# Kernel optimization log

Measured on AMD Instinct MI355X. Metric: run time of the kernel, lower is better.

## Reference

```python
import jax, jax.numpy as jnp
import numpy as np

IN_CH, IN_U, OUT_CH, OUT_U = 1152, 8, 10, 16
BATCH = 256
ROUTING_EPOCH = 3


def squash(s, axis=-1):
    # v = (||s||^2 / (1 + ||s||^2)) * s / ||s||
    sqn = jnp.sum(s * s, axis=axis, keepdims=True)
    return s * (sqn / ((1.0 + sqn) * jnp.sqrt(sqn + 1e-9)))


def setup_inputs() -> dict:
    key = jax.random.key(0)
    k1, k2 = jax.random.split(key)
    inp = jax.random.normal(k1, (BATCH, IN_CH, IN_U), dtype=jnp.float32)
    W = jax.random.normal(k2, (IN_CH, OUT_CH, OUT_U, IN_U), dtype=jnp.float32)
    return {"inp": inp, "W": W}


def reference(inp, W):
    # u_hat[b,i,o,u] = sum_k W[i,o,u,k] * inp[b,i,k]   -> [B, 1152, 10, 16]
    u_hat = jnp.einsum('iouk,bik->biou', W, inp)
    B = inp.shape[0]
    b = jnp.zeros((IN_CH, OUT_CH), dtype=inp.dtype)  # routing logits [1152, 10]
    v = None
    for _ in range(ROUTING_EPOCH):
        c = jax.nn.softmax(b, axis=1)                 # [1152, 10]
        s = jnp.einsum('biou,io->bou', u_hat, c)      # sum over input capsules -> [B, 10, 16]
        v = squash(s, axis=-1)                        # [B, 10, 16]
        # delta_b[i,o] = mean_b sum_u u_hat[b,i,o,u] * v[b,o,u]
        b = b + jnp.einsum('biou,bou->io', u_hat, v) / B
    return v  # == original v.squeeze(): [B, 10, 16]
```

## Files before the change

### kernel.cpp

```cpp
#include <hip/hip_runtime.h>
#include <math.h>

#define NB 256
#define IC 1152
#define OC 10
#define OU 16
#define IK 8
#define KTOT (IC * IK)
#define NTOT (OC * OU)
#define S_KS 16

typedef __attribute__((ext_vector_type(8))) short short8;
typedef __attribute__((ext_vector_type(4))) float f32x4;

static __device__ __forceinline__ unsigned short f2bf(float f) {
    unsigned u = __float_as_uint(f);
    unsigned r = (u + 0x7FFF + ((u >> 16) & 1)) >> 16;
    return (unsigned short)r;
}

__global__ __launch_bounds__(256) void prep_kernel(
    const float* __restrict__ inp,
    float* __restrict__ blog,
    unsigned short* __restrict__ inpb,
    unsigned short* __restrict__ inpT)
{
    const int kt  = blockIdx.x;
    const int bt  = blockIdx.y;
    const int tid = threadIdx.x;

    {
        int bid = blockIdx.y * 144 + blockIdx.x;
        if (bid < 45) blog[bid * 256 + tid] = 0.f;
    }

    __shared__ unsigned short sh[64][65];

#pragma unroll
    for (int j = 0; j < 4; ++j) {
        int q     = j * 256 + tid;
        int b_loc = q >> 4;
        int kq    = (q & 15) * 4;
        float4 g = *(const float4*)&inp[(size_t)(bt * 64 + b_loc) * KTOT + kt * 64 + kq];
        unsigned short h0 = f2bf(g.x), h1 = f2bf(g.y), h2 = f2bf(g.z), h3 = f2bf(g.w);
        sh[kq][b_loc] = h0; sh[kq + 1][b_loc] = h1;
        sh[kq + 2][b_loc] = h2; sh[kq + 3][b_loc] = h3;
        short4 pk = { (short)h0, (short)h1, (short)h2, (short)h3 };
        *(short4*)&inpb[(size_t)(bt * 64 + b_loc) * KTOT + kt * 64 + kq] = pk;
    }
    __syncthreads();

#pragma unroll
    for (int j = 0; j < 4; ++j) {
        int q     = j * 256 + tid;
        int k_loc = q >> 4;
        int b4    = (q & 15) * 4;
        short4 pk = { (short)sh[k_loc][b4],     (short)sh[k_loc][b4 + 1],
                      (short)sh[k_loc][b4 + 2], (short)sh[k_loc][b4 + 3] };
        *(short4*)&inpT[(size_t)(kt * 64 + k_loc) * 256 + bt * 64 + b4] = pk;
    }
}

#define BLP 584
__global__ __launch_bounds__(256) void spass_kernel(
    const unsigned short* __restrict__ inpb,
    const float* __restrict__ W,
    const float* __restrict__ blog,
    float* __restrict__ part)
{
    const int bid  = blockIdx.x;
    const int nt   = bid % 10;
    const int ks   = (bid / 10) % 16;
    const int mtg  = bid / 160;
    const int tid  = threadIdx.x;
    const int w    = tid >> 6;
    const int lane = tid & 63;
    const int l15  = lane & 15;
    const int koff = (lane >> 4) * 8;
    const int k0   = ks * 576;
    const int i0   = ks * 72;
    const int mt   = mtg * 4 + w;

    __shared__ unsigned short Bl[16 * BLP];
    __shared__ float c_loc[72];

    if (tid < 72) {
        const float* br = &blog[(size_t)(i0 + tid) * OC];
        float x[OC], m = -1e30f;
#pragma unroll
        for (int o = 0; o < OC; ++o) { x[o] = br[o]; m = fmaxf(m, x[o]); }
        float ssum = 0.f;
#pragma unroll
        for (int o = 0; o < OC; ++o) ssum += expf(x[o] - m);
        c_loc[tid] = expf(x[nt] - m) / ssum;
    }
    __syncthreads();

#pragma unroll
    for (int jj = 0; jj < 5; ++jj) {
        int q = jj * 256 + tid;
        if (q < 1152) {
            int i_loc = q >> 4, u = q & 15;
            const float* wr = W + (((size_t)(i0 + i_loc) * OC + nt) * OU + u) * IK;
            float4 a = *(const float4*)wr;
            float4 b = *(const float4*)(wr + 4);
            float cc = c_loc[i_loc];
            union { short8 v; unsigned short us[8]; } pk;
            pk.us[0] = f2bf(cc * a.x); pk.us[1] = f2bf(cc * a.y);
            pk.us[2] = f2bf(cc * a.z); pk.us[3] = f2bf(cc * a.w);
            pk.us[4] = f2bf(cc * b.x); pk.us[5] = f2bf(cc * b.y);
            pk.us[6] = f2bf(cc * b.z); pk.us[7] = f2bf(cc * b.w);
            *(short8*)&Bl[u * BLP + i_loc * 8] = pk.v;
        }
    }
    __syncthreads();

    const unsigned short* ap  = inpb + (size_t)(mt * 16 + l15) * KTOT + k0 + koff;
    const unsigned short* bls = &Bl[l15 * BLP + koff];

    f32x4 acc = {0.f, 0.f, 0.f, 0.f};
#pragma unroll
    for (int kk = 0; kk < 18; ++kk) {
        short8 av = *(const short8*)(ap + kk * 32);
        short8 bv = *(const short8*)(bls + kk * 32);
        acc = __builtin_amdgcn_mfma_f32_16x16x32_bf16(av, bv, acc, 0, 0, 0);
    }

    float* pp = part + ((size_t)ks * NB + mt * 16 + (lane >> 4) * 4) * NTOT + nt * 16 + l15;
#pragma unroll
    for (int r = 0; r < 4; ++r)
        pp[(size_t)r * NTOT] = acc[r];
}

__global__ __launch_bounds__(256) void reduce_squash_kernel(
    const float* __restrict__ part, float* __restrict__ vout,
    unsigned short* __restrict__ vT)
{
    const int tid = threadIdx.x;
    const int el  = tid & 31;
    const int kl  = tid >> 5;
    const int e   = blockIdx.x * 32 + el;

    float a = part[(size_t)(kl * 2) * (NB * NTOT) + e]
            + part[(size_t)(kl * 2 + 1) * (NB * NTOT) + e];

    __shared__ float red[8][36];
    red[kl][el] = a;
    __syncthreads();

    if (tid < 32) {
        float s = ((red[0][el] + red[1][el]) + (red[2][el] + red[3][el]))
                + ((red[4][el] + red[5][el]) + (red[6][el] + red[7][el]));
        float sq = s * s;
        sq += __shfl_xor(sq, 1);
        sq += __shfl_xor(sq, 2);
        sq += __shfl_xor(sq, 4);
        sq += __shfl_xor(sq, 8);
        float vv = s * (sq / ((1.f + sq) * sqrtf(sq + 1e-9f)));
        vout[e] = vv;
        int n = e % NTOT, b = e / NTOT;
        vT[(size_t)n * 256 + b] = f2bf(vv);
    }
}

__global__ __launch_bounds__(256) void delta_kernel(
    const unsigned short* __restrict__ inpT,
    const unsigned short* __restrict__ vT,
    const float* __restrict__ W,
    float* __restrict__ blog)
{
    const int g    = blockIdx.x * 4 + (threadIdx.x >> 6);
    const int lane = threadIdx.x & 63;
    const int mt   = g % 576;
    const int nt   = g / 576;
    const int l15  = lane & 15;
    const int quad = lane >> 4;
    const int koff = quad * 8;

    const unsigned short* ap = inpT + (size_t)(mt * 16 + l15) * 256 + koff;
    const unsigned short* bp = vT   + (size_t)(nt * 16 + l15) * 256 + koff;

    f32x4 acc = {0.f, 0.f, 0.f, 0.f};
#pragma unroll
    for (int kk = 0; kk < 8; ++kk) {
        short8 av = *(const short8*)(ap + kk * 32);
        short8 bv = *(const short8*)(bp + kk * 32);
        acc = __builtin_amdgcn_mfma_f32_16x16x32_bf16(av, bv, acc, 0, 0, 0);
    }

    const int i = mt * 2 + (quad >> 1);
    const float* wr = W + (((size_t)i * OC + nt) * OU + l15) * IK + (quad & 1) * 4;
    float4 wf = *(const float4*)wr;
    float wsum = wf.x * acc[0] + wf.y * acc[1] + wf.z * acc[2] + wf.w * acc[3];

    wsum += __shfl_xor(wsum, 16);
    wsum += __shfl_xor(wsum, 1);
    wsum += __shfl_xor(wsum, 2);
    wsum += __shfl_xor(wsum, 4);
    wsum += __shfl_xor(wsum, 8);

    if ((lane & 31) == 0)
        blog[(size_t)i * OC + nt] += wsum * (1.0f / NB);
}

extern "C" void kernel_launch(void* const* d_in, const int* in_sizes, int n_in,
                              void* d_out, int out_size, void* d_ws, size_t ws_size,
                              hipStream_t stream) {
    const float* inp = (const float*)d_in[0];
    const float* W   = (const float*)d_in[1];
    float* vout = (float*)d_out;

    float* blog = (float*)d_ws;
    float* part = blog + IC * OC;
    unsigned short* inpb = (unsigned short*)(part + (size_t)S_KS * NB * NTOT);
    unsigned short* inpT = inpb + (size_t)NB * KTOT;
    unsigned short* vT   = inpT + (size_t)KTOT * 256;

    prep_kernel<<<dim3(144, 4), dim3(256), 0, stream>>>(inp, blog, inpb, inpT);

    for (int t = 0; t < 3; ++t) {
        spass_kernel<<<dim3(640), dim3(256), 0, stream>>>(inpb, W, blog, part);
        reduce_squash_kernel<<<dim3(NB * NTOT / 32), dim3(256), 0, stream>>>(part, vout, vT);
        if (t < 2)
            delta_kernel<<<dim3(1440), dim3(256), 0, stream>>>(inpT, vT, W, blog);
    }
}
```

Baseline: 132.8 us.

## Fuse partial-sum reduction and squash into delta kernel for first two iterations

The delta kernel now reduces the split-K partial sums, applies squash, and builds the bf16 transposed v tile in shared memory itself, for its own output-capsule slice. This removes two reduce/squash launches and the global vT round trip. In exchange, each of the 36 blocks per output capsule recomputes the same reduction and squash, so part is read redundantly. Blocks grow to 1024 threads with extra shared memory.

```diff
diff --git a/kernel.cpp b/kernel.cpp
--- a/kernel.cpp
+++ b/kernel.cpp
@@ -133,8 +133,7 @@
 }
 
 __global__ __launch_bounds__(256) void reduce_squash_kernel(
-    const float* __restrict__ part, float* __restrict__ vout,
-    unsigned short* __restrict__ vT)
+    const float* __restrict__ part, float* __restrict__ vout)
 {
     const int tid = threadIdx.x;
     const int el  = tid & 31;
@@ -156,29 +155,69 @@
         sq += __shfl_xor(sq, 2);
         sq += __shfl_xor(sq, 4);
         sq += __shfl_xor(sq, 8);
-        float vv = s * (sq / ((1.f + sq) * sqrtf(sq + 1e-9f)));
-        vout[e] = vv;
-        int n = e % NTOT, b = e / NTOT;
-        vT[(size_t)n * 256 + b] = f2bf(vv);
-    }
-}
-
-__global__ __launch_bounds__(256) void delta_kernel(
+        vout[e] = s * (sq / ((1.f + sq) * sqrtf(sq + 1e-9f)));
+    }
+}
+
+__global__ __launch_bounds__(1024) void delta_fused_kernel(
+    const float* __restrict__ part,
     const unsigned short* __restrict__ inpT,
-    const unsigned short* __restrict__ vT,
     const float* __restrict__ W,
     float* __restrict__ blog)
 {
-    const int g    = blockIdx.x * 4 + (threadIdx.x >> 6);
-    const int lane = threadIdx.x & 63;
-    const int mt   = g % 576;
-    const int nt   = g / 576;
+    const int mtg = blockIdx.x;
+    const int nt  = blockIdx.y;
+    const int tid = threadIdx.x;
+
+    __shared__ float sred[256][17];
+    __shared__ float alpha[256];
+    __shared__ unsigned short vT_loc[16][264];
+
+    {
+        const int nl = tid & 15;
+        const int bq = tid >> 4;
+#pragma unroll
+        for (int rep = 0; rep < 4; ++rep) {
+            int b = bq + rep * 64;
+            const float* pp = part + (size_t)b * NTOT + nt * 16 + nl;
+            float s = 0.f;
+#pragma unroll
+            for (int ks = 0; ks < S_KS; ++ks)
+                s += pp[(size_t)ks * (NB * NTOT)];
+            sred[b][nl] = s;
+        }
+    }
+    __syncthreads();
+
+    if (tid < 256) {
+        const int b = tid;
+        float sq = 0.f;
+#pragma unroll
+        for (int u = 0; u < 16; ++u) { float x = sred[b][u]; sq += x * x; }
+        alpha[b] = sq / ((1.f + sq) * sqrtf(sq + 1e-9f));
+    }
+    __syncthreads();
+
+    {
+        const int nl = tid & 15;
+        const int bq = tid >> 4;
+#pragma unroll
+        for (int rep = 0; rep < 4; ++rep) {
+            int b = bq + rep * 64;
+            vT_loc[nl][b] = f2bf(sred[b][nl] * alpha[b]);
+        }
+    }
+    __syncthreads();
+
+    const int w    = tid >> 6;
+    const int lane = tid & 63;
+    const int mt   = mtg * 16 + w;
     const int l15  = lane & 15;
     const int quad = lane >> 4;
     const int koff = quad * 8;
 
     const unsigned short* ap = inpT + (size_t)(mt * 16 + l15) * 256 + koff;
-    const unsigned short* bp = vT   + (size_t)(nt * 16 + l15) * 256 + koff;
+    const unsigned short* bp = &vT_loc[l15][koff];
 
     f32x4 acc = {0.f, 0.f, 0.f, 0.f};
 #pragma unroll
@@ -214,14 +253,13 @@
     float* part = blog + IC * OC;
     unsigned short* inpb = (unsigned short*)(part + (size_t)S_KS * NB * NTOT);
     unsigned short* inpT = inpb + (size_t)NB * KTOT;
-    unsigned short* vT   = inpT + (size_t)KTOT * 256;
 
     prep_kernel<<<dim3(144, 4), dim3(256), 0, stream>>>(inp, blog, inpb, inpT);
 
-    for (int t = 0; t < 3; ++t) {
-        spass_kernel<<<dim3(640), dim3(256), 0, stream>>>(inpb, W, blog, part);
-        reduce_squash_kernel<<<dim3(NB * NTOT / 32), dim3(256), 0, stream>>>(part, vout, vT);
-        if (t < 2)
-            delta_kernel<<<dim3(1440), dim3(256), 0, stream>>>(inpT, vT, W, blog);
-    }
-}
+    spass_kernel<<<dim3(640), dim3(256), 0, stream>>>(inpb, W, blog, part);
+    delta_fused_kernel<<<dim3(36, 10), dim3(1024), 0, stream>>>(part, inpT, W, blog);
+    spass_kernel<<<dim3(640), dim3(256), 0, stream>>>(inpb, W, blog, part);
+    delta_fused_kernel<<<dim3(36, 10), dim3(1024), 0, stream>>>(part, inpT, W, blog);
+    spass_kernel<<<dim3(640), dim3(256), 0, stream>>>(inpb, W, blog, part);
+    reduce_squash_kernel<<<dim3(NB * NTOT / 32), dim3(256), 0, stream>>>(part, vout);
+}
```

Measured after the change: 157.6 us. 18.6% more time.

## Fuse split-K reduction and squash into spass via last-block atomic counter

Applied to the files above, without the earlier changes.

Removes the separate reduce_squash kernel. Each spass block atomically increments a per-tile counter, and the last of the 16 split-K blocks sums the partials, applies squash, and writes vout and vT. This saves three kernel launches and the extra pass over the partials, at the cost of a threadfence and an atomic per wave. Separate counter regions are zeroed in prep and used per iteration.

```diff
diff --git a/kernel.cpp b/kernel.cpp
--- a/kernel.cpp
+++ b/kernel.cpp
@@ -23,7 +23,8 @@
     const float* __restrict__ inp,
     float* __restrict__ blog,
     unsigned short* __restrict__ inpb,
-    unsigned short* __restrict__ inpT)
+    unsigned short* __restrict__ inpT,
+    int* __restrict__ cnt)
 {
     const int kt  = blockIdx.x;
     const int bt  = blockIdx.y;
@@ -32,6 +33,10 @@
     {
         int bid = blockIdx.y * 144 + blockIdx.x;
         if (bid < 45) blog[bid * 256 + tid] = 0.f;
+        if (bid >= 100 && bid < 102) {
+            int q = (bid - 100) * 256 + tid;
+            if (q < 480) cnt[q] = 0;
+        }
     }
 
     __shared__ unsigned short sh[64][65];
@@ -66,7 +71,10 @@
     const unsigned short* __restrict__ inpb,
     const float* __restrict__ W,
     const float* __restrict__ blog,
-    float* __restrict__ part)
+    float* __restrict__ part,
+    float* __restrict__ vout,
+    unsigned short* __restrict__ vT,
+    int* __restrict__ cnt)
 {
     const int bid  = blockIdx.x;
     const int nt   = bid % 10;
@@ -130,36 +138,33 @@
 #pragma unroll
     for (int r = 0; r < 4; ++r)
         pp[(size_t)r * NTOT] = acc[r];
-}
-
-__global__ __launch_bounds__(256) void reduce_squash_kernel(
-    const float* __restrict__ part, float* __restrict__ vout,
-    unsigned short* __restrict__ vT)
-{
-    const int tid = threadIdx.x;
-    const int el  = tid & 31;
-    const int kl  = tid >> 5;
-    const int e   = blockIdx.x * 32 + el;
-
-    float a = part[(size_t)(kl * 2) * (NB * NTOT) + e]
-            + part[(size_t)(kl * 2 + 1) * (NB * NTOT) + e];
-
-    __shared__ float red[8][36];
-    red[kl][el] = a;
-    __syncthreads();
-
-    if (tid < 32) {
-        float s = ((red[0][el] + red[1][el]) + (red[2][el] + red[3][el]))
-                + ((red[4][el] + red[5][el]) + (red[6][el] + red[7][el]));
-        float sq = s * s;
-        sq += __shfl_xor(sq, 1);
-        sq += __shfl_xor(sq, 2);
-        sq += __shfl_xor(sq, 4);
-        sq += __shfl_xor(sq, 8);
-        float vv = s * (sq / ((1.f + sq) * sqrtf(sq + 1e-9f)));
-        vout[e] = vv;
-        int n = e % NTOT, b = e / NTOT;
-        vT[(size_t)n * 256 + b] = f2bf(vv);
+
+    __threadfence();
+    int old = 0;
+    if (lane == 0) old = atomicAdd(&cnt[mt * 10 + nt], 1);
+    old = __shfl(old, 0);
+    if (old == S_KS - 1) {
+        __threadfence();
+        const int bl = l15;
+        const int ug = lane >> 4;
+        const float* pr = part + (size_t)(mt * 16 + bl) * NTOT + nt * 16 + ug * 4;
+        float4 s4 = {0.f, 0.f, 0.f, 0.f};
+#pragma unroll
+        for (int k2 = 0; k2 < S_KS; ++k2) {
+            float4 p4 = *(const float4*)(pr + (size_t)k2 * (NB * NTOT));
+            s4.x += p4.x; s4.y += p4.y; s4.z += p4.z; s4.w += p4.w;
+        }
+        float sq = s4.x * s4.x + s4.y * s4.y + s4.z * s4.z + s4.w * s4.w;
+        sq += __shfl_xor(sq, 16);
+        sq += __shfl_xor(sq, 32);
+        float alpha = sq / ((1.f + sq) * sqrtf(sq + 1e-9f));
+        float4 v4 = { s4.x * alpha, s4.y * alpha, s4.z * alpha, s4.w * alpha };
+        *(float4*)&vout[(size_t)(mt * 16 + bl) * NTOT + nt * 16 + ug * 4] = v4;
+        unsigned short* vt = vT + (size_t)(nt * 16 + ug * 4) * 256 + mt * 16 + bl;
+        vt[0]   = f2bf(v4.x);
+        vt[256] = f2bf(v4.y);
+        vt[512] = f2bf(v4.z);
+        vt[768] = f2bf(v4.w);
     }
 }
 
@@ -215,13 +220,13 @@
     unsigned short* inpb = (unsigned short*)(part + (size_t)S_KS * NB * NTOT);
     unsigned short* inpT = inpb + (size_t)NB * KTOT;
     unsigned short* vT   = inpT + (size_t)KTOT * 256;
-
-    prep_kernel<<<dim3(144, 4), dim3(256), 0, stream>>>(inp, blog, inpb, inpT);
-
-    for (int t = 0; t < 3; ++t) {
-        spass_kernel<<<dim3(640), dim3(256), 0, stream>>>(inpb, W, blog, part);
-        reduce_squash_kernel<<<dim3(NB * NTOT / 32), dim3(256), 0, stream>>>(part, vout, vT);
-        if (t < 2)
-            delta_kernel<<<dim3(1440), dim3(256), 0, stream>>>(inpT, vT, W, blog);
-    }
-}
+    int* cnt = (int*)(vT + (size_t)NTOT * 256);
+
+    prep_kernel<<<dim3(144, 4), dim3(256), 0, stream>>>(inp, blog, inpb, inpT, cnt);
+
+    spass_kernel<<<dim3(640), dim3(256), 0, stream>>>(inpb, W, blog, part, vout, vT, cnt);
+    delta_kernel<<<dim3(1440), dim3(256), 0, stream>>>(inpT, vT, W, blog);
+    spass_kernel<<<dim3(640), dim3(256), 0, stream>>>(inpb, W, blog, part, vout, vT, cnt + 160);
+    delta_kernel<<<dim3(1440), dim3(256), 0, stream>>>(inpT, vT, W, blog);
+    spass_kernel<<<dim3(640), dim3(256), 0, stream>>>(inpb, W, blog, part, vout, vT, cnt + 320);
+}
```

Measured after the change: 382.4 us. +187.9%, slower.
